# Kernel tuning notes

Measured on AMD Instinct MI355X. Metric: run time of the kernel, lower is better.

Reference implementation:

```python
import jax, jax.numpy as jnp
import numpy as np
import math

# dims
BSZ, L, D = 2, 4096, 1024
EXPAND, DS, NH, NG, DC, CS = 2, 128, 32, 1, 4, 64
DI = EXPAND * D            # 2048
HP = DI // NH              # 64 headdim
D_IN_PROJ = 2 * DI + 2 * NG * DS + NH  # 4384
CONV_DIM = DI + 2 * NG * DS            # 2304
EPS = 1e-5


def setup_inputs() -> dict:
    key = jax.random.key(0)
    ks = jax.random.split(key, 10)
    u = jax.random.normal(ks[0], (BSZ, L, D), dtype=jnp.float32)
    W_in = jax.random.normal(ks[1], (D, D_IN_PROJ), dtype=jnp.float32) / math.sqrt(D)
    conv_w = jax.random.normal(ks[2], (CONV_DIM, DC), dtype=jnp.float32) / math.sqrt(DC)
    conv_b = jnp.zeros((CONV_DIM,), dtype=jnp.float32)
    # dt init as in module: dt ~ logspace(1e-3, 0.1), dt_bias = inv softplus
    dt = jnp.exp(jax.random.uniform(ks[3], (NH,)) * (math.log(0.1) - math.log(0.001)) + math.log(0.001))
    dt = jnp.clip(dt, 1e-4, None)
    dt_bias = dt + jnp.log(-jnp.expm1(-dt))
    A_log = jnp.log(jax.random.uniform(ks[4], (NH,), minval=1.0, maxval=16.0))
    norm_w = jnp.ones((DI,), dtype=jnp.float32)
    norm_b = jnp.zeros((DI,), dtype=jnp.float32)
    W_out = jax.random.normal(ks[5], (DI, D), dtype=jnp.float32) / math.sqrt(DI)
    return {"u": u, "W_in": W_in, "conv_w": conv_w, "conv_b": conv_b,
            "dt_bias": dt_bias, "A_log": A_log, "norm_w": norm_w,
            "norm_b": norm_b, "W_out": W_out}


def _segsum(x):
    # x: (..., l) -> (..., l, l), out[i,j] = sum_{j<t<=i} x[t], -inf above diag
    cs = jnp.cumsum(x, axis=-1)
    d = cs[..., :, None] - cs[..., None, :]
    n = x.shape[-1]
    mask = jnp.tril(jnp.ones((n, n), dtype=bool))
    return jnp.where(mask, d, -jnp.inf)


def _ssd(x, A, Bm, Cm):
    # x: (b,l,h,p) already scaled by dt; A: (b,l,h) = a*dt; Bm,Cm: (b,l,h,n)
    b, l, h, p = x.shape
    nc = l // CS
    x = x.reshape(b, nc, CS, h, p)
    A = A.reshape(b, nc, CS, h).transpose(0, 3, 1, 2)          # (b,h,c,s)
    Bm = Bm.reshape(b, nc, CS, h, -1)
    Cm = Cm.reshape(b, nc, CS, h, -1)
    A_cum = jnp.cumsum(A, axis=-1)                              # (b,h,c,s)
    Lmat = jnp.exp(_segsum(A))                                  # (b,h,c,s,s)
    # intra-chunk (diagonal block) output
    Yd = jnp.einsum('bclhn,bcshn,bhcls,bcshp->bclhp', Cm, Bm, Lmat, x)
    # per-chunk final states
    decay_states = jnp.exp(A_cum[..., -1:] - A_cum)             # (b,h,c,s)
    states = jnp.einsum('bcshn,bhcs,bcshp->bchpn', Bm, decay_states, x)
    # inter-chunk recurrence (parallel via segsum over chunk decays)
    A_chunk = jnp.pad(A_cum[..., -1], ((0, 0), (0, 0), (1, 0)))  # (b,h,c+1)
    decay_chunk = jnp.exp(_segsum(A_chunk))                      # (b,h,c+1,c+1)
    states0 = jnp.concatenate([jnp.zeros_like(states[:, :1]), states], axis=1)
    new_states = jnp.einsum('bhzc,bchpn->bzhpn', decay_chunk, states0)
    states_in = new_states[:, :-1]                               # (b,c,h,p,n)
    state_decay = jnp.exp(A_cum)                                 # (b,h,c,s)
    Yoff = jnp.einsum('bcshn,bchpn,bhcs->bcshp', Cm, states_in, state_decay)
    return (Yd + Yoff).reshape(b, l, h, p)


def _causal_dwconv(x, w, b):
    # x: (B,L,C), depthwise causal conv, kernel w: (C,K), bias b: (C,)
    k = w.shape[1]
    xp = jnp.pad(x, ((0, 0), (k - 1, 0), (0, 0)))
    seqlen = x.shape[1]
    out = b
    for i in range(k):  # small fixed kernel loop (K=4)
        out = out + xp[:, i:i + seqlen, :] * w[:, i]
    return out


def reference(u, W_in, conv_w, conv_b, dt_bias, A_log, norm_w, norm_b, W_out):
    b, l, _ = u.shape
    zxbcdt = u @ W_in                                  # (b,l,2*DI+2*NG*DS+NH)
    z = zxbcdt[..., :DI]
    xBC = zxbcdt[..., DI:DI + CONV_DIM]
    dt = jax.nn.softplus(zxbcdt[..., -NH:] + dt_bias)  # (b,l,h)
    A = -jnp.exp(A_log)                                # (h,)
    xBC = jax.nn.silu(_causal_dwconv(xBC, conv_w, conv_b))
    x = xBC[..., :DI].reshape(b, l, NH, HP)
    Bv = xBC[..., DI:DI + NG * DS].reshape(b, l, NG, DS)
    Cv = xBC[..., DI + NG * DS:].reshape(b, l, NG, DS)
    # broadcast groups to heads
    rep = NH // NG
    Bh = jnp.repeat(Bv, rep, axis=2)                   # (b,l,h,n)
    Ch = jnp.repeat(Cv, rep, axis=2)
    y = _ssd(x * dt[..., None], A * dt, Bh, Ch)        # (b,l,h,p)
    y = y.reshape(b, l, DI)
    y = y * jax.nn.silu(z)                             # gated
    mu = jnp.mean(y, axis=-1, keepdims=True)
    var = jnp.mean(jnp.square(y - mu), axis=-1, keepdims=True)
    y = (y - mu) * jax.lax.rsqrt(var + EPS) * norm_w + norm_b
    return y @ W_out
```

## Files before the change

kernel.cpp:

```cpp
#include <hip/hip_runtime.h>
#include <hip/hip_bf16.h>
#include <math.h>


namespace {

constexpr int kB   = 2;
constexpr int kL   = 4096;
constexpr int kDI  = 2048;
constexpr int kDS  = 128;
constexpr int kNH  = 32;
constexpr int kHP  = 64;
constexpr int kDC  = 4;
constexpr int kCS  = 64;
constexpr int kNC  = kL / kCS;
constexpr int kDProj   = 2 * kDI + 2 * kDS + kNH;
constexpr int kDProjP  = 4480;
constexpr int kConvDim = kDI + 2 * kDS;
constexpr int kRows = kB * kL;
constexpr float kEps = 1e-5f;
constexpr int kTS = 136;
constexpr int kWS = 72;

typedef __bf16 bf16x8 __attribute__((ext_vector_type(8)));
typedef float f32x4 __attribute__((ext_vector_type(4)));
typedef unsigned short ushort8 __attribute__((ext_vector_type(8)));

__device__ inline float bu2f(unsigned short u) {
  union { unsigned int i; float f; } x; x.i = ((unsigned int)u) << 16; return x.f;
}
__device__ inline unsigned short f2bu(float f) {
  __hip_bfloat16 h = __float2bfloat16(f);
  return *reinterpret_cast<unsigned short*>(&h);
}

__device__ inline void store_out(float* C, size_t i, float v) { C[i] = v; }
__device__ inline void store_out(unsigned short* C, size_t i, float v) { C[i] = f2bu(v); }

__device__ inline void gld_lds16(const unsigned short* g, unsigned short* l) {
  __builtin_amdgcn_global_load_lds(
      (const __attribute__((address_space(1))) unsigned int*)g,
      (__attribute__((address_space(3))) unsigned int*)l, 16, 0, 0);
}

__global__ void cast_kernel(const float4* __restrict__ in, ushort4* __restrict__ out, int n4) {
  int i = blockIdx.x * 256 + threadIdx.x;
  if (i >= n4) return;
  float4 v = in[i];
  ushort4 o;
  o.x = f2bu(v.x); o.y = f2bu(v.y); o.z = f2bu(v.z); o.w = f2bu(v.w);
  out[i] = o;
}

__global__ void transpose_cast(const float* __restrict__ in, unsigned short* __restrict__ out,
                               int R, int C, const float* __restrict__ scale) {
  __shared__ float t[32][33];
  const int c0 = blockIdx.x * 32;
  const int r0 = blockIdx.y * 32;
  const int tx = threadIdx.x & 31, ty = threadIdx.x >> 5;
  for (int rr = ty; rr < 32; rr += 8) {
    int c = c0 + tx;
    float v = (c < C) ? in[(size_t)(r0 + rr) * C + c] : 0.f;
    if (scale) v *= scale[r0 + rr];
    t[rr][tx] = v;
  }
  __syncthreads();
  for (int cc = ty; cc < 32; cc += 8) {
    int orow = c0 + cc;
    out[(size_t)orow * R + r0 + tx] = f2bu(t[tx][cc]);
  }
}

__global__ void colsum_kernel(const float* __restrict__ W2, const float* __restrict__ wv,
                              const float* __restrict__ bv,
                              float* __restrict__ t1, float* __restrict__ t2) {
  __shared__ float p1[4][64], p2[4][64];
  const int nl = threadIdx.x & 63;
  const int ks = threadIdx.x >> 6;
  const int n = blockIdx.x * 64 + nl;
  float s1 = 0.f, s2 = 0.f;
  for (int k = ks * 512; k < ks * 512 + 512; k++) {
    float v = W2[(size_t)k * 1024 + n];
    s1 += wv[k] * v;
    s2 += bv[k] * v;
  }
  p1[ks][nl] = s1; p2[ks][nl] = s2;
  __syncthreads();
  if (threadIdx.x < 64) {
    t1[blockIdx.x * 64 + threadIdx.x] =
        p1[0][threadIdx.x] + p1[1][threadIdx.x] + p1[2][threadIdx.x] + p1[3][threadIdx.x];
    t2[blockIdx.x * 64 + threadIdx.x] =
        p2[0][threadIdx.x] + p2[1][threadIdx.x] + p2[2][threadIdx.x] + p2[3][threadIdx.x];
  }
}

template <typename OutT, bool FOLD>
__global__ __launch_bounds__(256) void gemm_bt(const unsigned short* __restrict__ A,
                                               const unsigned short* __restrict__ Bt,
                                               OutT* __restrict__ C, int M, int N, int K,
                                               const float* __restrict__ mu,
                                               const float* __restrict__ rstd,
                                               const float* __restrict__ t1,
                                               const float* __restrict__ t2) {
  __shared__ __align__(16) unsigned short As[128 * 32];
  __shared__ __align__(16) unsigned short Bs[128 * 32];
  const int tid = threadIdx.x;
  const int wave = tid >> 6, lane = tid & 63;
  const int m0 = blockIdx.y * 128, n0 = blockIdx.x * 128;
  const int wr = (wave >> 1) * 64, wc = (wave & 1) * 64;
  const int st_row = lane >> 2;
  const int st_col = (lane & 3) * 8;
  const unsigned short* pA[2];
  const unsigned short* pB[2];
  unsigned short* lA[2];
  unsigned short* lB[2];
#pragma unroll
  for (int r = 0; r < 2; r++) {
    int q = wave * 2 + r;
    pA[r] = A + (size_t)(m0 + q * 16 + st_row) * K + st_col;
    pB[r] = Bt + (size_t)(n0 + q * 16 + st_row) * K + st_col;
    lA[r] = &As[q * 512];
    lB[r] = &Bs[q * 512];
  }
  const int frag_row = lane & 15;
  const int frag_k = (lane >> 4) * 8;
  f32x4 acc[4][4] = {};
  for (int k0 = 0; k0 < K; k0 += 32) {
#pragma unroll
    for (int r = 0; r < 2; r++) {
      gld_lds16(pA[r] + k0, lA[r]);
      gld_lds16(pB[r] + k0, lB[r]);
    }
    asm volatile("s_waitcnt vmcnt(0)" ::: "memory");
    __syncthreads();
    bf16x8 af[4], bfr[4];
#pragma unroll
    for (int i = 0; i < 4; i++)
      af[i] = *(const bf16x8*)&As[(wr + i * 16 + frag_row) * 32 + frag_k];
#pragma unroll
    for (int j = 0; j < 4; j++)
      bfr[j] = *(const bf16x8*)&Bs[(wc + j * 16 + frag_row) * 32 + frag_k];
#pragma unroll
    for (int i = 0; i < 4; i++)
#pragma unroll
      for (int j = 0; j < 4; j++)
        acc[i][j] = __builtin_amdgcn_mfma_f32_16x16x32_bf16(af[i], bfr[j], acc[i][j], 0, 0, 0);
    __syncthreads();
  }
  const int crow = (lane >> 4) * 4;
  const int ccol = lane & 15;
#pragma unroll
  for (int i = 0; i < 4; i++) {
#pragma unroll
    for (int j = 0; j < 4; j++) {
      int n = n0 + wc + j * 16 + ccol;
      if (n < N) {
        float c1 = FOLD ? t1[n] : 0.f;
        float c2 = FOLD ? t2[n] : 0.f;
#pragma unroll
        for (int r = 0; r < 4; r++) {
          int m = m0 + wr + i * 16 + crow + r;
          float v = acc[i][j][r];
          if (FOLD) v = rstd[m] * (v - mu[m] * c1) + c2;
          store_out(C, (size_t)m * N + n, v);
        }
      }
    }
  }
}

__global__ void dt_kernel(const unsigned short* __restrict__ zxbcdt,
                          const float* __restrict__ dt_bias,
                          float* __restrict__ dtbuf) {
  int idx = blockIdx.x * 256 + threadIdx.x;
  if (idx >= kRows * kNH) return;
  int row = idx >> 5, h = idx & 31;
  float x = bu2f(zxbcdt[(size_t)row * kDProj + (kDProj - kNH) + h]) + dt_bias[h];
  dtbuf[idx] = (x > 15.f) ? x : log1pf(expf(x));
}

__global__ void conv_silu_kernel(const unsigned short* __restrict__ zxbcdt,
                                 const float* __restrict__ conv_w,
                                 const float* __restrict__ conv_b,
                                 unsigned short* __restrict__ xbc_act) {
  int c = blockIdx.x * 256 + threadIdx.x;
  if (c >= kConvDim) return;
  const int r0 = blockIdx.y * 8;
  const int l0 = r0 & (kL - 1);
  const float w0 = conv_w[c * 4], w1 = conv_w[c * 4 + 1];
  const float w2 = conv_w[c * 4 + 2], w3 = conv_w[c * 4 + 3];
  const float bias = conv_b[c];
  float v[11];
#pragma unroll
  for (int i = 0; i < 11; i++) {
    int l = l0 - 3 + i;
    v[i] = (l >= 0) ? bu2f(zxbcdt[(size_t)(r0 - 3 + i) * kDProj + kDI + c]) : 0.f;
  }
#pragma unroll
  for (int j = 0; j < 8; j++) {
    float a = bias + v[j] * w0 + v[j + 1] * w1 + v[j + 2] * w2 + v[j + 3] * w3;
    xbc_act[(size_t)(r0 + j) * kConvDim + c] = f2bu(a / (1.f + expf(-a)));
  }
}

__global__ __launch_bounds__(256) void chunk_state_kernel(
    const unsigned short* __restrict__ xbc_act,
    const float* __restrict__ dtbuf,
    const float* __restrict__ A_log,
    unsigned short* __restrict__ states,
    float* __restrict__ asum) {
  const int id = blockIdx.x;
  const int h = id & 31;
  const int c = (id >> 5) & (kNC - 1);
  const int b = id >> 11;
  const int tid = threadIdx.x;
  const int wave = tid >> 6, lane = tid & 63;
  __shared__ __align__(16) unsigned short sBT[kDS * kWS];
  __shared__ __align__(16) unsigned short sxd[kCS * kWS];
  __shared__ float s_dt[kCS];
  __shared__ float s_acum[kCS];
  const int l0 = b * kL + c * kCS;
  if (tid < kCS) s_dt[tid] = dtbuf[(size_t)(l0 + tid) * kNH + h];
  __syncthreads();
  if (tid == 0) {
    float A = -expf(A_log[h]);
    float run = 0.f;
    for (int s = 0; s < kCS; s++) { run += A * s_dt[s]; s_acum[s] = run; }
    asum[id] = run;
  }
  __syncthreads();
  const float total = s_acum[kCS - 1];
  for (int e = tid; e < kCS * kDS; e += 256) {
    int s = e >> 7, n = e & 127;
    sBT[n * kWS + s] = xbc_act[(size_t)(l0 + s) * kConvDim + kDI + n];
  }
  for (int e = tid; e < kCS * kHP; e += 256) {
    int s = e >> 6, p = e & 63;
    float xv = bu2f(xbc_act[(size_t)(l0 + s) * kConvDim + h * kHP + p]);
    sxd[p * kWS + s] = f2bu(xv * s_dt[s] * expf(total - s_acum[s]));
  }
  __syncthreads();
  const int arow = wave * 16 + (lane & 15);
  const int fk = (lane >> 4) * 8;
  f32x4 acc[8] = {};
#pragma unroll
  for (int kk = 0; kk < 2; kk++) {
    bf16x8 a = *(const bf16x8*)&sxd[arow * kWS + kk * 32 + fk];
#pragma unroll
    for (int j = 0; j < 8; j++) {
      bf16x8 bb = *(const bf16x8*)&sBT[(j * 16 + (lane & 15)) * kWS + kk * 32 + fk];
      acc[j] = __builtin_amdgcn_mfma_f32_16x16x32_bf16(a, bb, acc[j], 0, 0, 0);
    }
  }
  const int prow = wave * 16 + (lane >> 4) * 4;
  const int ncol = lane & 15;
  size_t base = (size_t)id * (kHP * kDS);
#pragma unroll
  for (int j = 0; j < 8; j++)
#pragma unroll
    for (int r = 0; r < 4; r++)
      states[base + (size_t)(prow + r) * kDS + j * 16 + ncol] = f2bu(acc[j][r]);
}

__global__ void scan_kernel(unsigned short* __restrict__ states,
                            const float* __restrict__ asum) {
  const int blk = blockIdx.x;
  const int seg = blk & 7;
  const int bh = blk >> 3;
  const int h = bh & 31, b = bh >> 5;
  const int e4 = seg * 256 + threadIdx.x;
  float c0 = 0.f, c1 = 0.f, c2 = 0.f, c3 = 0.f;
  for (int c = 0; c < kNC; c++) {
    const int id = (b * kNC + c) * kNH + h;
    ushort4* p = (ushort4*)states + (size_t)id * 2048 + e4;
    float decay = expf(asum[id]);
    ushort4 t = *p;
    ushort4 o;
    o.x = f2bu(c0); o.y = f2bu(c1); o.z = f2bu(c2); o.w = f2bu(c3);
    *p = o;
    c0 = c0 * decay + bu2f(t.x);
    c1 = c1 * decay + bu2f(t.y);
    c2 = c2 * decay + bu2f(t.z);
    c3 = c3 * decay + bu2f(t.w);
  }
}

__global__ __launch_bounds__(256) void y_kernel(
    const unsigned short* __restrict__ xbc_act,
    const unsigned short* __restrict__ zxbcdt,
    const unsigned short* __restrict__ states_in,
    const float* __restrict__ dtbuf,
    const float* __restrict__ A_log,
    unsigned short* __restrict__ ybuf) {
  const int id = blockIdx.x;
  const int hg = id & 7;
  const int c = (id >> 3) & (kNC - 1);
  const int b = id >> 9;
  const int tid = threadIdx.x;
  const int wave = tid >> 6, lane = tid & 63;
  __shared__ __align__(16) unsigned short sC[kCS * kTS];
  __shared__ __align__(16) unsigned short sB[kCS * kTS];
  __shared__ __align__(16) unsigned short sxd[kCS * kWS];
  __shared__ __align__(16) unsigned short sW[kCS * kWS];
  __shared__ float s_dt[4][kCS];
  __shared__ float s_acum[4][kCS];
  const int l0 = b * kL + c * kCS;
  {
    int hh = tid >> 6, s = tid & 63;
    s_dt[hh][s] = dtbuf[(size_t)(l0 + s) * kNH + hg * 4 + hh];
  }
  __syncthreads();
  if (tid < 4) {
    float A = -expf(A_log[hg * 4 + tid]);
    float run = 0.f;
    for (int s = 0; s < kCS; s++) { run += A * s_dt[tid][s]; s_acum[tid][s] = run; }
  }
  for (int e = tid; e < kCS * 16; e += 256) {
    int row = e >> 4, c8 = (e & 15) * 8;
    size_t rb = (size_t)(l0 + row) * kConvDim;
    *(ushort8*)&sB[row * kTS + c8] = *(const ushort8*)&xbc_act[rb + kDI + c8];
    *(ushort8*)&sC[row * kTS + c8] = *(const ushort8*)&xbc_act[rb + kDI + kDS + c8];
  }
  __syncthreads();
  const int arow = wave * 16 + (lane & 15);
  const int fk = (lane >> 4) * 8;
  f32x4 accG[4] = {};
#pragma unroll
  for (int kk = 0; kk < 4; kk++) {
    bf16x8 a = *(const bf16x8*)&sC[arow * kTS + kk * 32 + fk];
#pragma unroll
    for (int j = 0; j < 4; j++) {
      bf16x8 bb = *(const bf16x8*)&sB[(j * 16 + (lane & 15)) * kTS + kk * 32 + fk];
      accG[j] = __builtin_amdgcn_mfma_f32_16x16x32_bf16(a, bb, accG[j], 0, 0, 0);
    }
  }
  const int lrow = wave * 16 + (lane >> 4) * 4;
  const size_t sbase = (size_t)((b * kNC + c) * kNH) * (kHP * kDS);
  for (int hh = 0; hh < 4; hh++) {
    const int h = hg * 4 + hh;
    __syncthreads();
    for (int e = tid; e < kCS * kHP; e += 256) {
      int s = e >> 6, p = e & 63;
      float xv = bu2f(xbc_act[(size_t)(l0 + s) * kConvDim + h * kHP + p]);
      sxd[p * kWS + s] = f2bu(xv * s_dt[hh][s]);
    }
#pragma unroll
    for (int j = 0; j < 4; j++) {
      int scol = j * 16 + (lane & 15);
      float as = s_acum[hh][scol];
#pragma unroll
      for (int r = 0; r < 4; r++) {
        int l = lrow + r;
        float w = (scol <= l) ? accG[j][r] * expf(s_acum[hh][l] - as) : 0.f;
        sW[l * kWS + scol] = f2bu(w);
      }
    }
    for (int e = tid; e < kCS * 16; e += 256) {
      int row = e >> 4, c8 = (e & 15) * 8;
      *(ushort8*)&sB[row * kTS + c8] =
          *(const ushort8*)&states_in[sbase + (size_t)h * (kHP * kDS) + row * kDS + c8];
    }
    __syncthreads();
    f32x4 accY[4] = {};
#pragma unroll
    for (int kk = 0; kk < 2; kk++) {
      bf16x8 a = *(const bf16x8*)&sW[arow * kWS + kk * 32 + fk];
#pragma unroll
      for (int j = 0; j < 4; j++) {
        bf16x8 bb = *(const bf16x8*)&sxd[(j * 16 + (lane & 15)) * kWS + kk * 32 + fk];
        accY[j] = __builtin_amdgcn_mfma_f32_16x16x32_bf16(a, bb, accY[j], 0, 0, 0);
      }
    }
    f32x4 accO[4] = {};
#pragma unroll
    for (int kk = 0; kk < 4; kk++) {
      bf16x8 a = *(const bf16x8*)&sC[arow * kTS + kk * 32 + fk];
#pragma unroll
      for (int j = 0; j < 4; j++) {
        bf16x8 bb = *(const bf16x8*)&sB[(j * 16 + (lane & 15)) * kTS + kk * 32 + fk];
        accO[j] = __builtin_amdgcn_mfma_f32_16x16x32_bf16(a, bb, accO[j], 0, 0, 0);
      }
    }
#pragma unroll
    for (int r = 0; r < 4; r++) {
      int l = lrow + r;
      float el = expf(s_acum[hh][l]);
      size_t zrow = (size_t)(l0 + l) * kDProj + h * kHP;
      size_t yrow = (size_t)(l0 + l) * kDI + h * kHP;
#pragma unroll
      for (int j = 0; j < 4; j++) {
        int p = j * 16 + (lane & 15);
        float yv = accY[j][r] + el * accO[j][r];
        float z = bu2f(zxbcdt[zrow + p]);
        yv *= z / (1.f + expf(-z));
        ybuf[yrow + p] = f2bu(yv);
      }
    }
  }
}

__global__ void rowstat_kernel(const unsigned short* __restrict__ y,
                               float* __restrict__ mu, float* __restrict__ rstd) {
  const int row = blockIdx.x;
  const unsigned short* yr = y + (size_t)row * kDI;
  float s = 0.f, ss = 0.f;
  for (int i = threadIdx.x; i < kDI; i += 256) {
    float v = bu2f(yr[i]);
    s += v; ss += v * v;
  }
#pragma unroll
  for (int off = 32; off > 0; off >>= 1) {
    s += __shfl_down(s, off);
    ss += __shfl_down(ss, off);
  }
  __shared__ float red[8];
  int lane = threadIdx.x & 63, wv = threadIdx.x >> 6;
  if (lane == 0) { red[wv] = s; red[4 + wv] = ss; }
  __syncthreads();
  if (threadIdx.x == 0) {
    float S = red[0] + red[1] + red[2] + red[3];
    float SS = red[4] + red[5] + red[6] + red[7];
    float m = S / kDI;
    float var = SS / kDI - m * m;
    mu[row] = m;
    rstd[row] = rsqrtf(var + kEps);
  }
}

}

extern "C" void kernel_launch(void* const* d_in, const int* in_sizes, int n_in,
                              void* d_out, int out_size, void* d_ws, size_t ws_size,
                              hipStream_t stream) {
  const float* u       = (const float*)d_in[0];
  const float* W_in    = (const float*)d_in[1];
  const float* conv_w  = (const float*)d_in[2];
  const float* conv_b  = (const float*)d_in[3];
  const float* dt_bias = (const float*)d_in[4];
  const float* A_log   = (const float*)d_in[5];
  const float* norm_w  = (const float*)d_in[6];
  const float* norm_b  = (const float*)d_in[7];
  const float* W_out   = (const float*)d_in[8];
  float* out = (float*)d_out;

  char* ws = (char*)d_ws;
  size_t off = 0;
  auto alloc = [&](size_t bytes) {
    void* p = ws + off;
    off += (bytes + 255) & ~(size_t)255;
    return p;
  };
  unsigned short* zxbcdt = (unsigned short*)alloc((size_t)kRows * kDProj * 2);
  unsigned short* xbc    = (unsigned short*)alloc((size_t)kRows * kConvDim * 2);
  float* dtb             = (float*)alloc((size_t)kRows * kNH * 4);
  float* asum            = (float*)alloc((size_t)kB * kNC * kNH * 4);
  unsigned short* A1     = (unsigned short*)alloc((size_t)kRows * 1024 * 2);
  unsigned short* Bt1    = (unsigned short*)alloc((size_t)kDProjP * 1024 * 2);
  unsigned short* states = (unsigned short*)alloc((size_t)kB * kNC * kNH * kHP * kDS * 2);
  unsigned short* Bt2    = (unsigned short*)alloc((size_t)1024 * kDI * 2);
  unsigned short* ybuf   = (unsigned short*)alloc((size_t)kRows * kDI * 2);
  float* mu              = (float*)alloc((size_t)kRows * 4);
  float* rstd            = (float*)alloc((size_t)kRows * 4);
  float* t1              = (float*)alloc(1024 * 4);
  float* t2              = (float*)alloc(1024 * 4);
  (void)ws_size; (void)in_sizes; (void)n_in; (void)out_size;

  cast_kernel<<<(kRows * 1024 / 4 + 255) / 256, 256, 0, stream>>>(
      (const float4*)u, (ushort4*)A1, kRows * 1024 / 4);
  transpose_cast<<<dim3(kDProjP / 32, 1024 / 32), 256, 0, stream>>>(
      W_in, Bt1, 1024, kDProj, nullptr);
  transpose_cast<<<dim3(1024 / 32, 2048 / 32), 256, 0, stream>>>(
      W_out, Bt2, 2048, 1024, norm_w);
  colsum_kernel<<<16, 256, 0, stream>>>(W_out, norm_w, norm_b, t1, t2);
  gemm_bt<unsigned short, false><<<dim3(kDProjP / 128, kRows / 128), 256, 0, stream>>>(
      A1, Bt1, zxbcdt, kRows, kDProj, 1024, nullptr, nullptr, nullptr, nullptr);
  dt_kernel<<<(kRows * kNH + 255) / 256, 256, 0, stream>>>(zxbcdt, dt_bias, dtb);
  conv_silu_kernel<<<dim3((kConvDim + 255) / 256, kRows / 8), 256, 0, stream>>>(
      zxbcdt, conv_w, conv_b, xbc);
  chunk_state_kernel<<<kB * kNC * kNH, 256, 0, stream>>>(xbc, dtb, A_log, states, asum);
  scan_kernel<<<kB * kNH * 8, 256, 0, stream>>>(states, asum);
  y_kernel<<<kB * kNC * 8, 256, 0, stream>>>(xbc, zxbcdt, states, dtb, A_log, ybuf);
  rowstat_kernel<<<kRows, 256, 0, stream>>>(ybuf, mu, rstd);
  gemm_bt<float, true><<<dim3(1024 / 128, kRows / 128), 256, 0, stream>>>(
      ybuf, Bt2, out, kRows, 1024, 2048, mu, rstd, t1, t2);
}
```

Measured before the change: 476.9 us.

## Swizzle GEMM LDS layout and fuse layernorm row stats into y_kernel

Applies an XOR swizzle to the k-offset of the GEMM shared-memory tiles, both when staging and when reading fragments, to reduce LDS bank conflicts. It also accumulates per-row sum and sum-of-squares of the gated output inside y_kernel, reduces them across lanes, and writes partials per head-group. A tiny ln_reduce kernel then combines these partials, replacing the rowstat kernel that re-read the full y buffer. The cost is extra registers and shuffles in y_kernel. Statistics are computed from fp32 values rather than the bf16-rounded ones.

```diff
diff --git a/kernel.cpp b/kernel.cpp
--- a/kernel.cpp
+++ b/kernel.cpp
@@ -109,7 +109,7 @@
   const int m0 = blockIdx.y * 128, n0 = blockIdx.x * 128;
   const int wr = (wave >> 1) * 64, wc = (wave & 1) * 64;
   const int st_row = lane >> 2;
-  const int st_col = (lane & 3) * 8;
+  const int st_col = (((lane & 3) ^ ((st_row >> 1) & 3))) * 8;
   const unsigned short* pA[2];
   const unsigned short* pB[2];
   unsigned short* lA[2];
@@ -123,7 +123,7 @@
     lB[r] = &Bs[q * 512];
   }
   const int frag_row = lane & 15;
-  const int frag_k = (lane >> 4) * 8;
+  const int rk = (((lane >> 4) ^ ((frag_row >> 1) & 3))) * 8;
   f32x4 acc[4][4] = {};
   for (int k0 = 0; k0 < K; k0 += 32) {
 #pragma unroll
@@ -136,10 +136,10 @@
     bf16x8 af[4], bfr[4];
 #pragma unroll
     for (int i = 0; i < 4; i++)
-      af[i] = *(const bf16x8*)&As[(wr + i * 16 + frag_row) * 32 + frag_k];
+      af[i] = *(const bf16x8*)&As[(wr + i * 16 + frag_row) * 32 + rk];
 #pragma unroll
     for (int j = 0; j < 4; j++)
-      bfr[j] = *(const bf16x8*)&Bs[(wc + j * 16 + frag_row) * 32 + frag_k];
+      bfr[j] = *(const bf16x8*)&Bs[(wc + j * 16 + frag_row) * 32 + rk];
 #pragma unroll
     for (int i = 0; i < 4; i++)
 #pragma unroll
@@ -291,7 +291,8 @@
     const unsigned short* __restrict__ states_in,
     const float* __restrict__ dtbuf,
     const float* __restrict__ A_log,
-    unsigned short* __restrict__ ybuf) {
+    unsigned short* __restrict__ ybuf,
+    float* __restrict__ pS, float* __restrict__ pQ) {
   const int id = blockIdx.x;
   const int hg = id & 7;
   const int c = (id >> 3) & (kNC - 1);
@@ -336,6 +337,7 @@
   }
   const int lrow = wave * 16 + (lane >> 4) * 4;
   const size_t sbase = (size_t)((b * kNC + c) * kNH) * (kHP * kDS);
+  float rS[4] = {}, rQ[4] = {};
   for (int hh = 0; hh < 4; hh++) {
     const int h = hg * 4 + hh;
     __syncthreads();
@@ -393,38 +395,40 @@
         float yv = accY[j][r] + el * accO[j][r];
         float z = bu2f(zxbcdt[zrow + p]);
         yv *= z / (1.f + expf(-z));
+        rS[r] += yv;
+        rQ[r] += yv * yv;
         ybuf[yrow + p] = f2bu(yv);
       }
     }
   }
-}
-
-__global__ void rowstat_kernel(const unsigned short* __restrict__ y,
-                               float* __restrict__ mu, float* __restrict__ rstd) {
-  const int row = blockIdx.x;
-  const unsigned short* yr = y + (size_t)row * kDI;
-  float s = 0.f, ss = 0.f;
-  for (int i = threadIdx.x; i < kDI; i += 256) {
-    float v = bu2f(yr[i]);
-    s += v; ss += v * v;
-  }
-#pragma unroll
-  for (int off = 32; off > 0; off >>= 1) {
-    s += __shfl_down(s, off);
-    ss += __shfl_down(ss, off);
-  }
-  __shared__ float red[8];
-  int lane = threadIdx.x & 63, wv = threadIdx.x >> 6;
-  if (lane == 0) { red[wv] = s; red[4 + wv] = ss; }
-  __syncthreads();
-  if (threadIdx.x == 0) {
-    float S = red[0] + red[1] + red[2] + red[3];
-    float SS = red[4] + red[5] + red[6] + red[7];
-    float m = S / kDI;
-    float var = SS / kDI - m * m;
-    mu[row] = m;
-    rstd[row] = rsqrtf(var + kEps);
-  }
+#pragma unroll
+  for (int m = 1; m < 16; m <<= 1) {
+#pragma unroll
+    for (int r = 0; r < 4; r++) {
+      rS[r] += __shfl_xor(rS[r], m);
+      rQ[r] += __shfl_xor(rQ[r], m);
+    }
+  }
+  if ((lane & 15) == 0) {
+#pragma unroll
+    for (int r = 0; r < 4; r++) {
+      int row = l0 + lrow + r;
+      pS[(size_t)row * 8 + hg] = rS[r];
+      pQ[(size_t)row * 8 + hg] = rQ[r];
+    }
+  }
+}
+
+__global__ void ln_reduce(const float* __restrict__ pS, const float* __restrict__ pQ,
+                          float* __restrict__ mu, float* __restrict__ rstd) {
+  int row = blockIdx.x * 256 + threadIdx.x;
+  if (row >= kRows) return;
+  float s = 0.f, q = 0.f;
+#pragma unroll
+  for (int i = 0; i < 8; i++) { s += pS[(size_t)row * 8 + i]; q += pQ[(size_t)row * 8 + i]; }
+  float m = s / kDI;
+  mu[row] = m;
+  rstd[row] = rsqrtf(q / kDI - m * m + kEps);
 }
 
 }
@@ -463,6 +467,8 @@
   float* rstd            = (float*)alloc((size_t)kRows * 4);
   float* t1              = (float*)alloc(1024 * 4);
   float* t2              = (float*)alloc(1024 * 4);
+  float* pS              = (float*)alloc((size_t)kRows * 8 * 4);
+  float* pQ              = (float*)alloc((size_t)kRows * 8 * 4);
   (void)ws_size; (void)in_sizes; (void)n_in; (void)out_size;
 
   cast_kernel<<<(kRows * 1024 / 4 + 255) / 256, 256, 0, stream>>>(
@@ -479,8 +485,8 @@
       zxbcdt, conv_w, conv_b, xbc);
   chunk_state_kernel<<<kB * kNC * kNH, 256, 0, stream>>>(xbc, dtb, A_log, states, asum);
   scan_kernel<<<kB * kNH * 8, 256, 0, stream>>>(states, asum);
-  y_kernel<<<kB * kNC * 8, 256, 0, stream>>>(xbc, zxbcdt, states, dtb, A_log, ybuf);
-  rowstat_kernel<<<kRows, 256, 0, stream>>>(ybuf, mu, rstd);
+  y_kernel<<<kB * kNC * 8, 256, 0, stream>>>(xbc, zxbcdt, states, dtb, A_log, ybuf, pS, pQ);
+  ln_reduce<<<kRows / 256, 256, 0, stream>>>(pS, pQ, mu, rstd);
   gemm_bt<float, true><<<dim3(1024 / 128, kRows / 128), 256, 0, stream>>>(
       ybuf, Bt2, out, kRows, 1024, 2048, mu, rstd, t1, t2);
 }
```

New measurement: 457.7 us. 4.0% less time.
